# Performance work log

Measured on AMD Instinct MI355X. Metric: run time of the kernel, lower is better.

Reference implementation:

```python
import jax, jax.numpy as jnp
import numpy as np

NUM_EMBEDDINGS = 128
EMBEDDING_DIM = 256
COMMITMENT_COST = 0.25
B, T = 64, 2048


def setup_inputs() -> dict:
    key = jax.random.key(0)
    k1, k2 = jax.random.split(key)
    inputs = jax.random.normal(k1, (B, T, EMBEDDING_DIM), dtype=jnp.float32)
    # codebook initialized like nn.Embedding weight (uniform in torch, normal fine for baseline)
    embedding = jax.random.normal(k2, (NUM_EMBEDDINGS, EMBEDDING_DIM), dtype=jnp.float32)
    return {"inputs": inputs, "embedding": embedding}


def reference(inputs, embedding):
    # eval-mode VectorQuantizerEMA.forward
    input_shape = inputs.shape
    flat = inputs.reshape(-1, EMBEDDING_DIM)                      # [N, D]
    distances = (
        jnp.sum(flat * flat, axis=1, keepdims=True)
        + jnp.sum(embedding * embedding, axis=1)
        - 2.0 * jnp.matmul(flat, embedding.T)
    )
    encoding_indices = jnp.argmin(distances, axis=1)              # [N]
    encodings = jax.nn.one_hot(encoding_indices, NUM_EMBEDDINGS, dtype=inputs.dtype)  # [N, K]
    quantized = embedding[encoding_indices].reshape(input_shape)  # gather lookup

    e_latent_loss = jnp.mean((jax.lax.stop_gradient(quantized) - inputs) ** 2)
    loss = COMMITMENT_COST * e_latent_loss

    # straight-through estimator
    quantized_st = inputs + jax.lax.stop_gradient(quantized - inputs)

    avg_probs = jnp.mean(encodings, axis=0)
    perplexity = jnp.exp(-jnp.sum(avg_probs * jnp.log(avg_probs + 1e-10)))

    encoding_indices = encoding_indices.reshape(input_shape[0], input_shape[1])
    return (loss, quantized_st, perplexity, encodings, encoding_indices)
```

## Files before the change

### kernel.cpp

```cpp
#include <hip/hip_runtime.h>
#include <math.h>

#define NUM_K 128
#define DIM   256
#define NROWS (64 * 2048)
#define BLOCK 256
#define ROWS_PER_BLOCK 64
#define GRID  (NROWS / ROWS_PER_BLOCK)

#define OFF_LOSS 0u
#define OFF_Q    1u
#define OFF_PERP 33554433u
#define OFF_ENC  33554434u
#define OFF_IDX  50331650u


typedef float f8v __attribute__((ext_vector_type(8)));

__global__ void vq_init(const float* __restrict__ E, float* __restrict__ ws) {
    int k = blockIdx.x, lane = threadIdx.x;
    float4 v = *(const float4*)(E + (size_t)k * DIM + lane * 4);
    float s = v.x * v.x + v.y * v.y + v.z * v.z + v.w * v.w;
    #pragma unroll
    for (int off = 32; off; off >>= 1) s += __shfl_down(s, off);
    if (lane == 0) ws[256 + k] = s;
    if (k == 0) {
        if (lane == 0) ws[0] = 0.0f;
        ((int*)ws)[64 + lane]  = 0;
        ((int*)ws)[128 + lane] = 0;
    }
}

__global__ __launch_bounds__(BLOCK, 4) void vq_main(
        const float* __restrict__ X, const float* __restrict__ E,
        float* ws, float* __restrict__ out) {
    const int tid  = threadIdx.x;
    const int lane = tid & 63;
    const int kg   = __builtin_amdgcn_readfirstlane(tid >> 6);
    const int r0   = blockIdx.x * ROWS_PER_BLOCK;
    const int row  = r0 + lane;
    const float* xrow = X + (size_t)row * DIM;
    const float* Eb   = E + (size_t)kg * 32 * DIM;

    f8v acc0, acc1, acc2, acc3;
    #pragma unroll
    for (int k = 0; k < 8; ++k) { acc0[k] = 0.f; acc1[k] = 0.f; acc2[k] = 0.f; acc3[k] = 0.f; }
    float sx = 0.0f;

    for (int dc = 0; dc < DIM; dc += 8) {
        float4 a0 = *(const float4*)(xrow + dc);
        float4 a1 = *(const float4*)(xrow + dc + 4);
        if (kg == 0) {
            sx = fmaf(a0.x, a0.x, sx); sx = fmaf(a0.y, a0.y, sx);
            sx = fmaf(a0.z, a0.z, sx); sx = fmaf(a0.w, a0.w, sx);
            sx = fmaf(a1.x, a1.x, sx); sx = fmaf(a1.y, a1.y, sx);
            sx = fmaf(a1.z, a1.z, sx); sx = fmaf(a1.w, a1.w, sx);
        }
#define KBODY(AC, KB)                                                     \
        _Pragma("unroll")                                                 \
        for (int k = 0; k < 8; ++k) {                                     \
            const float* er = Eb + (size_t)(KB + k) * DIM + dc;           \
            AC[k] = fmaf(a0.x, er[0], AC[k]);                             \
            AC[k] = fmaf(a0.y, er[1], AC[k]);                             \
            AC[k] = fmaf(a0.z, er[2], AC[k]);                             \
            AC[k] = fmaf(a0.w, er[3], AC[k]);                             \
            AC[k] = fmaf(a1.x, er[4], AC[k]);                             \
            AC[k] = fmaf(a1.y, er[5], AC[k]);                             \
            AC[k] = fmaf(a1.z, er[6], AC[k]);                             \
            AC[k] = fmaf(a1.w, er[7], AC[k]);                             \
        }
        KBODY(acc0, 0)
        KBODY(acc1, 8)
        KBODY(acc2, 16)
        KBODY(acc3, 24)
#undef KBODY
    }

    const float* se = ws + 256 + kg * 32;
    float dmin = INFINITY; int idx = kg * 32;
#define AMIN(AC, KB)                                                      \
    _Pragma("unroll")                                                     \
    for (int k = 0; k < 8; ++k) {                                         \
        float t = se[KB + k] - 2.0f * AC[k];                              \
        if (t < dmin) { dmin = t; idx = kg * 32 + KB + k; }               \
    }
    AMIN(acc0, 0) AMIN(acc1, 8) AMIN(acc2, 16) AMIN(acc3, 24)
#undef AMIN

    __shared__ float rd[4][ROWS_PER_BLOCK];
    __shared__ int   ri[4][ROWS_PER_BLOCK];
    __shared__ float rsx[ROWS_PER_BLOCK];
    __shared__ int   idxs[ROWS_PER_BLOCK];
    __shared__ int   hcnt[NUM_K];
    rd[kg][lane] = dmin;
    ri[kg][lane] = idx;
    if (kg == 0) rsx[lane] = sx;
    if (tid < NUM_K) hcnt[tid] = 0;
    __syncthreads();

    if (kg == 0) {
        float dm = rd[0][lane]; int ix = ri[0][lane];
        #pragma unroll
        for (int g = 1; g < 4; ++g) {
            float t = rd[g][lane];
            if (t < dm) { dm = t; ix = ri[g][lane]; }
        }
        idxs[lane] = ix;
        out[OFF_IDX + row] = (float)ix;
        atomicAdd(&hcnt[ix], 1);
        float v = rsx[lane] + dm;
        #pragma unroll
        for (int off = 32; off; off >>= 1) v += __shfl_down(v, off);
        if (lane == 0) atomicAdd(&ws[0], v);
    }
    __syncthreads();
    if (tid < NUM_K && hcnt[tid]) atomicAdd((int*)ws + 64 + tid, hcnt[tid]);

    for (int r = 0; r < ROWS_PER_BLOCK; ++r) {
        int ix = idxs[r];
        out[OFF_Q + (size_t)(r0 + r) * DIM + tid] = E[(size_t)ix * DIM + tid];
    }
    for (int it = 0; it < 16; ++it) {
        int s  = it * BLOCK + tid;
        int r  = s >> 6;
        int kp = (s & 63) * 2;
        int ix = idxs[r];
        float2 e2;
        e2.x = (kp     == ix) ? 1.0f : 0.0f;
        e2.y = (kp + 1 == ix) ? 1.0f : 0.0f;
        *(float2*)(out + OFF_ENC + (size_t)(r0 + r) * NUM_K + kp) = e2;
    }
}

__global__ void vq_final(const float* __restrict__ ws, float* __restrict__ out) {
    int t = threadIdx.x;
    if (t == 0) out[OFF_LOSS] = 0.25f * (ws[0] / (float)((size_t)NROWS * DIM));
    int c = ((const int*)ws)[64 + t];
    float p = (float)c / (float)NROWS;
    float v = p * logf(p + 1e-10f);
    #pragma unroll
    for (int off = 32; off; off >>= 1) v += __shfl_down(v, off);
    __shared__ float red[2];
    if ((t & 63) == 0) red[t >> 6] = v;
    __syncthreads();
    if (t == 0) out[OFF_PERP] = expf(-(red[0] + red[1]));
}

extern "C" void kernel_launch(void* const* d_in, const int* in_sizes, int n_in,
                              void* d_out, int out_size, void* d_ws, size_t ws_size,
                              hipStream_t stream) {
    const float* X = (const float*)d_in[0];
    const float* E = (const float*)d_in[1];
    float* out = (float*)d_out;
    float* ws  = (float*)d_ws;

    vq_init <<<NUM_K, 64, 0, stream>>>(E, ws);
    vq_main <<<GRID, BLOCK, 0, stream>>>(X, E, ws, out);
    vq_final<<<1, 128, 0, stream>>>(ws, out);
}
```

Baseline: 404.2 us.

## Compute distances with split-bf16 MFMA emulating fp32 and widen output stores

Replaces the scalar FMA distance matmul with MFMA 16x16x32 bf16 instructions, splitting each fp32 operand into three bf16 pieces and summing six cross products to approximate fp32 accuracy. Rows per block grow to 128, each wave handles a 32-code slice, and an xor-shuffle argmin with index tie-break reduces within each wave. The quantized and one-hot stores are widened to float4. The aim is to cut the ALU-bound dot-product cost, in exchange for extra split/pack work, more registers, and a risk of argmin mismatches on near-ties.

```diff
diff --git a/kernel.cpp b/kernel.cpp
--- a/kernel.cpp
+++ b/kernel.cpp
@@ -5,8 +5,8 @@
 #define DIM   256
 #define NROWS (64 * 2048)
 #define BLOCK 256
-#define ROWS_PER_BLOCK 64
-#define GRID  (NROWS / ROWS_PER_BLOCK)
+#define RPB   128
+#define GRID  (NROWS / RPB)
 
 #define OFF_LOSS 0u
 #define OFF_Q    1u
@@ -15,7 +15,34 @@
 #define OFF_IDX  50331650u
 
 
-typedef float f8v __attribute__((ext_vector_type(8)));
+typedef __attribute__((ext_vector_type(8))) short bf16x8;
+typedef __attribute__((ext_vector_type(4))) float f32x4;
+typedef float f4a __attribute__((ext_vector_type(4), aligned(4)));
+
+union PackU { uint4 u; bf16x8 v; };
+
+__device__ __forceinline__ bf16x8 pack_hi16(const unsigned int* w) {
+  PackU p;
+  p.u.x = (w[1] & 0xFFFF0000u) | (w[0] >> 16);
+  p.u.y = (w[3] & 0xFFFF0000u) | (w[2] >> 16);
+  p.u.z = (w[5] & 0xFFFF0000u) | (w[4] >> 16);
+  p.u.w = (w[7] & 0xFFFF0000u) | (w[6] >> 16);
+  return p.v;
+}
+
+__device__ __forceinline__ void split3(const float* xf, bf16x8& a, bf16x8& b, bf16x8& c) {
+  unsigned int ua[8], ub[8], uc[8];
+  #pragma unroll
+  for (int i = 0; i < 8; ++i) {
+    float x = xf[i];
+    unsigned int ha = __float_as_uint(x) & 0xFFFF0000u;
+    float r1 = x - __uint_as_float(ha);
+    unsigned int hb = __float_as_uint(r1) & 0xFFFF0000u;
+    float r2 = r1 - __uint_as_float(hb);
+    ua[i] = ha; ub[i] = hb; uc[i] = __float_as_uint(r2);
+  }
+  a = pack_hi16(ua); b = pack_hi16(ub); c = pack_hi16(uc);
+}
 
 __global__ void vq_init(const float* __restrict__ E, float* __restrict__ ws) {
     int k = blockIdx.x, lane = threadIdx.x;
@@ -31,104 +58,151 @@
     }
 }
 
-__global__ __launch_bounds__(BLOCK, 4) void vq_main(
+__global__ __launch_bounds__(BLOCK, 2) void vq_main(
         const float* __restrict__ X, const float* __restrict__ E,
         float* ws, float* __restrict__ out) {
     const int tid  = threadIdx.x;
     const int lane = tid & 63;
     const int kg   = __builtin_amdgcn_readfirstlane(tid >> 6);
-    const int r0   = blockIdx.x * ROWS_PER_BLOCK;
-    const int row  = r0 + lane;
-    const float* xrow = X + (size_t)row * DIM;
-    const float* Eb   = E + (size_t)kg * 32 * DIM;
-
-    f8v acc0, acc1, acc2, acc3;
-    #pragma unroll
-    for (int k = 0; k < 8; ++k) { acc0[k] = 0.f; acc1[k] = 0.f; acc2[k] = 0.f; acc3[k] = 0.f; }
+    const int l4   = lane & 15;
+    const int g    = lane >> 4;
+    const int r0   = blockIdx.x * RPB;
+
+    __shared__ float rd[4][RPB];
+    __shared__ int   ri[4][RPB];
+    __shared__ int   idxs[RPB];
+    __shared__ int   hcnt[NUM_K];
+    if (tid < NUM_K) hcnt[tid] = 0;
+
+    const float* xp = X + (size_t)(r0 + l4) * DIM + g * 8;
+    const float* ep = E + (size_t)(kg * 32 + l4) * DIM + g * 8;
+
+    f32x4 acc[8][2];
+    #pragma unroll
+    for (int rt = 0; rt < 8; ++rt) {
+        acc[rt][0] = (f32x4)0.0f;
+        acc[rt][1] = (f32x4)0.0f;
+    }
     float sx = 0.0f;
 
-    for (int dc = 0; dc < DIM; dc += 8) {
-        float4 a0 = *(const float4*)(xrow + dc);
-        float4 a1 = *(const float4*)(xrow + dc + 4);
-        if (kg == 0) {
-            sx = fmaf(a0.x, a0.x, sx); sx = fmaf(a0.y, a0.y, sx);
-            sx = fmaf(a0.z, a0.z, sx); sx = fmaf(a0.w, a0.w, sx);
-            sx = fmaf(a1.x, a1.x, sx); sx = fmaf(a1.y, a1.y, sx);
-            sx = fmaf(a1.z, a1.z, sx); sx = fmaf(a1.w, a1.w, sx);
-        }
-#define KBODY(AC, KB)                                                     \
-        _Pragma("unroll")                                                 \
-        for (int k = 0; k < 8; ++k) {                                     \
-            const float* er = Eb + (size_t)(KB + k) * DIM + dc;           \
-            AC[k] = fmaf(a0.x, er[0], AC[k]);                             \
-            AC[k] = fmaf(a0.y, er[1], AC[k]);                             \
-            AC[k] = fmaf(a0.z, er[2], AC[k]);                             \
-            AC[k] = fmaf(a0.w, er[3], AC[k]);                             \
-            AC[k] = fmaf(a1.x, er[4], AC[k]);                             \
-            AC[k] = fmaf(a1.y, er[5], AC[k]);                             \
-            AC[k] = fmaf(a1.z, er[6], AC[k]);                             \
-            AC[k] = fmaf(a1.w, er[7], AC[k]);                             \
-        }
-        KBODY(acc0, 0)
-        KBODY(acc1, 8)
-        KBODY(acc2, 16)
-        KBODY(acc3, 24)
-#undef KBODY
-    }
-
-    const float* se = ws + 256 + kg * 32;
-    float dmin = INFINITY; int idx = kg * 32;
-#define AMIN(AC, KB)                                                      \
-    _Pragma("unroll")                                                     \
-    for (int k = 0; k < 8; ++k) {                                         \
-        float t = se[KB + k] - 2.0f * AC[k];                              \
-        if (t < dmin) { dmin = t; idx = kg * 32 + KB + k; }               \
-    }
-    AMIN(acc0, 0) AMIN(acc1, 8) AMIN(acc2, 16) AMIN(acc3, 24)
-#undef AMIN
-
-    __shared__ float rd[4][ROWS_PER_BLOCK];
-    __shared__ int   ri[4][ROWS_PER_BLOCK];
-    __shared__ float rsx[ROWS_PER_BLOCK];
-    __shared__ int   idxs[ROWS_PER_BLOCK];
-    __shared__ int   hcnt[NUM_K];
-    rd[kg][lane] = dmin;
-    ri[kg][lane] = idx;
-    if (kg == 0) rsx[lane] = sx;
-    if (tid < NUM_K) hcnt[tid] = 0;
+    #pragma unroll 1
+    for (int half = 0; half < 2; ++half) {
+        const int kbase = half * 128;
+        bf16x8 ea[2][4], eb[2][4], ec[2][4];
+        #pragma unroll
+        for (int ct = 0; ct < 2; ++ct) {
+            #pragma unroll
+            for (int ch = 0; ch < 4; ++ch) {
+                const float* p = ep + (size_t)ct * 16 * DIM + kbase + ch * 32;
+                float4 v0 = *(const float4*)(p);
+                float4 v1 = *(const float4*)(p + 4);
+                float xf[8] = {v0.x, v0.y, v0.z, v0.w, v1.x, v1.y, v1.z, v1.w};
+                split3(xf, ea[ct][ch], eb[ct][ch], ec[ct][ch]);
+            }
+        }
+        #pragma unroll
+        for (int rt = 0; rt < 8; ++rt) {
+            #pragma unroll
+            for (int ch = 0; ch < 4; ++ch) {
+                const float* p = xp + (size_t)rt * 16 * DIM + kbase + ch * 32;
+                float4 v0 = *(const float4*)(p);
+                float4 v1 = *(const float4*)(p + 4);
+                float xf[8] = {v0.x, v0.y, v0.z, v0.w, v1.x, v1.y, v1.z, v1.w};
+                if (kg == 0) {
+                    #pragma unroll
+                    for (int i = 0; i < 8; ++i) sx = fmaf(xf[i], xf[i], sx);
+                }
+                bf16x8 xa, xb, xc;
+                split3(xf, xa, xb, xc);
+                acc[rt][0] = __builtin_amdgcn_mfma_f32_16x16x32_bf16(xa, ea[0][ch], acc[rt][0], 0, 0, 0);
+                acc[rt][1] = __builtin_amdgcn_mfma_f32_16x16x32_bf16(xa, ea[1][ch], acc[rt][1], 0, 0, 0);
+                acc[rt][0] = __builtin_amdgcn_mfma_f32_16x16x32_bf16(xa, eb[0][ch], acc[rt][0], 0, 0, 0);
+                acc[rt][1] = __builtin_amdgcn_mfma_f32_16x16x32_bf16(xa, eb[1][ch], acc[rt][1], 0, 0, 0);
+                acc[rt][0] = __builtin_amdgcn_mfma_f32_16x16x32_bf16(xb, ea[0][ch], acc[rt][0], 0, 0, 0);
+                acc[rt][1] = __builtin_amdgcn_mfma_f32_16x16x32_bf16(xb, ea[1][ch], acc[rt][1], 0, 0, 0);
+                acc[rt][0] = __builtin_amdgcn_mfma_f32_16x16x32_bf16(xa, ec[0][ch], acc[rt][0], 0, 0, 0);
+                acc[rt][1] = __builtin_amdgcn_mfma_f32_16x16x32_bf16(xa, ec[1][ch], acc[rt][1], 0, 0, 0);
+                acc[rt][0] = __builtin_amdgcn_mfma_f32_16x16x32_bf16(xc, ea[0][ch], acc[rt][0], 0, 0, 0);
+                acc[rt][1] = __builtin_amdgcn_mfma_f32_16x16x32_bf16(xc, ea[1][ch], acc[rt][1], 0, 0, 0);
+                acc[rt][0] = __builtin_amdgcn_mfma_f32_16x16x32_bf16(xb, eb[0][ch], acc[rt][0], 0, 0, 0);
+                acc[rt][1] = __builtin_amdgcn_mfma_f32_16x16x32_bf16(xb, eb[1][ch], acc[rt][1], 0, 0, 0);
+            }
+        }
+        __syncthreads();
+    }
+
+    const float* sep = ws + 256 + kg * 32;
+    const float se0 = sep[l4];
+    const float se1 = sep[l4 + 16];
+    const int   c0  = kg * 32 + l4;
+
+    #pragma unroll
+    for (int rt = 0; rt < 8; ++rt) {
+        #pragma unroll
+        for (int r = 0; r < 4; ++r) {
+            float t0 = fmaf(-2.0f, acc[rt][0][r], se0);
+            float t1 = fmaf(-2.0f, acc[rt][1][r], se1);
+            float t; int ci;
+            if (t1 < t0) { t = t1; ci = c0 + 16; } else { t = t0; ci = c0; }
+            #pragma unroll
+            for (int m = 1; m <= 8; m <<= 1) {
+                float tv = __shfl_xor(t, m);
+                int   cv = __shfl_xor(ci, m);
+                if (tv < t || (tv == t && cv < ci)) { t = tv; ci = cv; }
+            }
+            if (l4 == 0) {
+                int rl = rt * 16 + g * 4 + r;
+                rd[kg][rl] = t;
+                ri[kg][rl] = ci;
+            }
+        }
+    }
+
+    if (kg == 0) {
+        #pragma unroll
+        for (int m = 1; m <= 32; m <<= 1) sx += __shfl_xor(sx, m);
+        if (lane == 0) atomicAdd(&ws[0], sx);
+    }
     __syncthreads();
 
-    if (kg == 0) {
-        float dm = rd[0][lane]; int ix = ri[0][lane];
-        #pragma unroll
-        for (int g = 1; g < 4; ++g) {
-            float t = rd[g][lane];
-            if (t < dm) { dm = t; ix = ri[g][lane]; }
-        }
-        idxs[lane] = ix;
-        out[OFF_IDX + row] = (float)ix;
+    if (tid < RPB) {
+        float dm = rd[0][tid]; int ix = ri[0][tid];
+        #pragma unroll
+        for (int gg = 1; gg < 4; ++gg) {
+            float t = rd[gg][tid];
+            if (t < dm) { dm = t; ix = ri[gg][tid]; }
+        }
+        idxs[tid] = ix;
+        out[OFF_IDX + r0 + tid] = (float)ix;
         atomicAdd(&hcnt[ix], 1);
-        float v = rsx[lane] + dm;
-        #pragma unroll
-        for (int off = 32; off; off >>= 1) v += __shfl_down(v, off);
-        if (lane == 0) atomicAdd(&ws[0], v);
+        float v = dm;
+        #pragma unroll
+        for (int m = 1; m <= 32; m <<= 1) v += __shfl_xor(v, m);
+        if ((tid & 63) == 0) atomicAdd(&ws[0], v);
     }
     __syncthreads();
     if (tid < NUM_K && hcnt[tid]) atomicAdd((int*)ws + 64 + tid, hcnt[tid]);
 
-    for (int r = 0; r < ROWS_PER_BLOCK; ++r) {
+    #pragma unroll 4
+    for (int it = 0; it < 32; ++it) {
+        int r  = it * 4 + (tid >> 6);
         int ix = idxs[r];
-        out[OFF_Q + (size_t)(r0 + r) * DIM + tid] = E[(size_t)ix * DIM + tid];
-    }
+        float4 v = *(const float4*)(E + (size_t)ix * DIM + (tid & 63) * 4);
+        f4a w = {v.x, v.y, v.z, v.w};
+        *(f4a*)(out + OFF_Q + (size_t)(r0 + r) * DIM + (tid & 63) * 4) = w;
+    }
+    #pragma unroll 4
     for (int it = 0; it < 16; ++it) {
         int s  = it * BLOCK + tid;
-        int r  = s >> 6;
-        int kp = (s & 63) * 2;
+        int r  = s >> 5;
+        int c4 = (s & 31) * 4;
         int ix = idxs[r];
-        float2 e2;
-        e2.x = (kp     == ix) ? 1.0f : 0.0f;
-        e2.y = (kp + 1 == ix) ? 1.0f : 0.0f;
-        *(float2*)(out + OFF_ENC + (size_t)(r0 + r) * NUM_K + kp) = e2;
+        f4a e4;
+        e4.x = (c4     == ix) ? 1.0f : 0.0f;
+        e4.y = (c4 + 1 == ix) ? 1.0f : 0.0f;
+        e4.z = (c4 + 2 == ix) ? 1.0f : 0.0f;
+        e4.w = (c4 + 3 == ix) ? 1.0f : 0.0f;
+        *(f4a*)(out + OFF_ENC + (size_t)(r0 + r) * NUM_K + c4) = e4;
     }
 }
 
```

Result: slower. 423.2 us (+4.7%).
